# Performance work log

Measured on AMD Instinct MI355X. Metric: run time of the kernel, lower is better.

Reference implementation:

```python
import jax, jax.numpy as jnp
import numpy as np

# static problem sizes (uniform graphs -> fully vectorizable index construction)
B = 1024          # graph pairs
QS, CS, MSS = 15, 18, 20   # query size, corpus size, max_set_size
NEW = CS - QS              # nodes added to each query ('Adding' variant)
QE, CE, NE = 40, 50, QS * NEW  # edges per query / corpus / new edges per pair
D, TD = 128, 16            # node_state_dim, transform_dim
P, T = 5, 3                # n_prop_layers, n_time_updates
NPP = 2 * CS               # nodes per pair after growth (query grown to CS)
N = B * NPP                # total nodes = 36864
E = B * (QE + CE + NE)     # total edges = 138240
SINKHORN_ITERS, SINKHORN_TEMP = 10, 0.1


def setup_inputs() -> dict:
    rng = np.random.default_rng(0)
    q_off = (np.arange(B) * NPP)[:, None]
    c_off = q_off + CS
    # original query/corpus edges (already shifted to post-growth global ids)
    qf = rng.integers(0, QS, (B, QE)) + q_off
    qt = rng.integers(0, QS, (B, QE)) + q_off
    cf = rng.integers(0, CS, (B, CE)) + c_off
    ct = rng.integers(0, CS, (B, CE)) + c_off
    # new all-pairs edges existing-query-node -> new-node
    nf_ = np.tile(np.repeat(np.arange(QS), NEW), (B, 1)) + q_off
    nt_ = np.tile(np.tile(np.arange(QS, CS), QS), (B, 1)) + q_off
    from_idx = jnp.asarray(np.concatenate([qf, cf, nf_], 1).ravel(), jnp.int32)
    to_idx = jnp.asarray(np.concatenate([qt, ct, nt_], 1).ravel(), jnp.int32)
    mult_factor = jnp.asarray(
        np.concatenate([np.ones((B, QE + CE)), np.zeros((B, NE))], 1).ravel(),
        jnp.float32)
    ks = jax.random.split(jax.random.key(0), 10)
    p = lambda k, shp: jax.random.normal(k, shp, jnp.float32) * 0.05
    z = lambda n: jnp.zeros((n,), jnp.float32)
    return dict(
        node_features=jnp.ones((N, 1), jnp.float32),
        edge_features=jnp.ones((E, 1), jnp.float32),
        mult_factor=mult_factor,
        W_ne=p(ks[0], (1, D)), b_ne=z(D),
        W_ee=p(ks[1], (1, D)), b_ee=z(D),
        W_m1=p(ks[2], (3 * D, 2 * D)), b_m1=z(2 * D),
        W_m2=p(ks[3], (2 * D, D)), b_m2=z(D),
        W_u1=p(ks[4], (2 * D, 2 * D)), b_u1=z(2 * D),
        W_u2=p(ks[5], (2 * D, D)), b_u2=z(D),
        W_c1=p(ks[6], (2 * D, 2 * D)), b_c1=z(2 * D),
        W_c2=p(ks[7], (2 * D, D)), b_c2=z(D),
        W_t1=p(ks[8], (D, TD)), b_t1=z(TD),
        W_t2=p(ks[9], (TD, TD)), b_t2=z(TD),
        from_idx=from_idx, to_idx=to_idx)


def _sinkhorn(log_alpha):
    la = log_alpha / SINKHORN_TEMP
    for _ in range(SINKHORN_ITERS):
        la = la - jax.nn.logsumexp(la, axis=2, keepdims=True)
        la = la - jax.nn.logsumexp(la, axis=1, keepdims=True)
    return jnp.exp(la)


def _forward(node_features, edge_features, mult_factor,
             W_ne, b_ne, W_ee, b_ee, W_m1, b_m1, W_m2, b_m2,
             W_u1, b_u1, W_u2, b_u2, W_c1, b_c1, W_c2, b_c2,
             W_t1, b_t1, W_t2, b_t2, from_idx, to_idx):
    relu = jax.nn.relu
    nf_enc = node_features @ W_ne + b_ne          # [N, D]
    ef_enc = edge_features @ W_ee + b_ee          # [E, D]
    store = jnp.zeros((N, D * (P + 1)), nf_enc.dtype)
    qmask = (jnp.arange(MSS) < QS).astype(nf_enc.dtype)[None, :, None]
    cmask = (jnp.arange(MSS) < CS).astype(nf_enc.dtype)[None, :, None]
    for _t in range(T):
        h = nf_enc
        blocks = [jnp.zeros((N, D), nf_enc.dtype)]
        for p_ in range(1, P + 1):
            inter = store[:, D * (p_ - 1):D * p_]
            comb = relu(jnp.concatenate([h, inter], 1) @ W_c1 + b_c1) @ W_c2 + b_c2
            # GraphPropLayer: message MLP over edges, masked segment-sum aggregate
            msg_in = jnp.concatenate([comb[from_idx], comb[to_idx], ef_enc], 1)
            msg = relu(msg_in @ W_m1 + b_m1) @ W_m2 + b_m2
            msg = msg * mult_factor[:, None]      # zero out added edges
            agg = jax.ops.segment_sum(msg, to_idx, num_segments=N)
            h = relu(jnp.concatenate([comb, agg], 1) @ W_u1 + b_u1) @ W_u2 + b_u2
            blocks.append(h)
        store = jnp.concatenate(blocks, 1)        # [N, D*(P+1)]
        # pad per-graph to max_set_size and split query/corpus (interleaved)
        stacked = store.reshape(2 * B, CS, D * (P + 1))
        stacked = jnp.pad(stacked, ((0, 0), (0, MSS - CS), (0, 0)))
        q_store, c_store = stacked[0::2], stacked[1::2]   # [B, MSS, D*(P+1)]
        q_fin, c_fin = q_store[:, :, -D:], c_store[:, :, -D:]
        tq = relu(q_fin @ W_t1 + b_t1) @ W_t2 + b_t2
        tc = relu(c_fin @ W_t1 + b_t1) @ W_t2 + b_t2
        mq, mc = tq * qmask, tc * cmask
        plan = _sinkhorn(jnp.einsum('bqt,bct->bqc', mq, mc))  # [B, MSS, MSS]
        q_from_c = jnp.einsum('bqc,bcf->bqf', plan, c_store)
        c_from_q = jnp.einsum('bqc,bqf->bcf', plan, q_store)
        inter_all = jnp.stack([q_from_c, c_from_q], 1).reshape(2 * B, MSS, -1)
        store = inter_all[:, :CS, :].reshape(N, D * (P + 1))
    score = -jnp.sum(relu(mq - jnp.einsum('bqc,bct->bqt', plan, mc)), axis=(1, 2))
    return score


def reference(node_features, edge_features, mult_factor,
              W_ne, b_ne, W_ee, b_ee, W_m1, b_m1, W_m2, b_m2,
              W_u1, b_u1, W_u2, b_u2, W_c1, b_c1, W_c2, b_c2,
              W_t1, b_t1, W_t2, b_t2, from_idx, to_idx):
    return _forward(node_features, edge_features, mult_factor,
                    W_ne, b_ne, W_ee, b_ee, W_m1, b_m1, W_m2, b_m2,
                    W_u1, b_u1, W_u2, b_u2, W_c1, b_c1, W_c2, b_c2,
                    W_t1, b_t1, W_t2, b_t2, from_idx, to_idx)
```

## Files before the change

### kernel.cpp

```cpp
#include <hip/hip_runtime.h>

#define Bq   1024
#define NQS  15
#define NCS  18
#define NMSS 20
#define NPPc 36
#define NN   36864
#define DD   128
#define NTD  16
#define NP   5
#define NT   3
#define NBLK 512

typedef __attribute__((ext_vector_type(8))) short short8;
typedef __attribute__((ext_vector_type(4))) short short4v;
typedef __attribute__((ext_vector_type(4))) float float4v;

__device__ __forceinline__ short f2bf(float f) {
  unsigned u = __builtin_bit_cast(unsigned, f);
  u = u + 0x7FFFu + ((u >> 16) & 1u);
  return (short)(u >> 16);
}
__device__ __forceinline__ float bf2f(short s) {
  unsigned u = ((unsigned)(unsigned short)s) << 16;
  return __builtin_bit_cast(float, u);
}

__device__ __forceinline__ int hs_idx(int row, int col) {
  return (row << 8) + ((((col >> 3) ^ (row & 7)) << 3) | (col & 7));
}
__device__ __forceinline__ int as_idx(int row, int col) {
  return (row << 7) + ((((col >> 3) ^ (row & 7)) << 3) | (col & 7));
}
__device__ __forceinline__ int ms_idx(int f, int e) {
  return f * 104 + e;
}

#define OFF_ACT 49152
#define OFF_AGG 67584
#define OFF_UNI 86016
#define OFF_FR  122880
#define OFF_TO  123648
#define OFF_EF  124416

struct MP {
  const float* node_f; const float* edge_f;
  const int* from_idx; const int* to_idx;
  const short *WTc1, *WTm1, *WTu1, *WTc2, *WTm2, *WTu2;
  const float *b_c1, *b_c2, *b_m1, *b_m2, *b_u1, *b_u2;
  const float *c_n, *d_n, *c_e, *d_e;
  const float *W_t1, *b_t1, *W_t2, *b_t2;
  short* blkg;
  short* mixg;
  float* out;
};

template<int MT, typename F>
__device__ __forceinline__ void gemm_full(const short* __restrict__ WT, F loadB,
                                          int wm, int quad, int l16, float4v (&acc)[MT][6]) {
  short8 afr[MT][8];
#pragma unroll
  for (int ks = 0; ks < 8; ++ks)
#pragma unroll
    for (int mt = 0; mt < MT; ++mt)
      afr[mt][ks] = *(const short8*)(WT + (long)(wm * (MT * 16) + mt * 16 + l16) * 256
                                        + ks * 32 + quad * 8);
#pragma unroll
  for (int mt = 0; mt < MT; ++mt)
#pragma unroll
    for (int nt = 0; nt < 6; ++nt) acc[mt][nt] = (float4v)0.f;
#pragma unroll
  for (int ks = 0; ks < 8; ++ks) {
    const int k0q = ks * 32 + quad * 8;
    short8 bfr[6];
#pragma unroll
    for (int nt = 0; nt < 6; ++nt) bfr[nt] = loadB(nt, k0q);
#pragma unroll
    for (int mt = 0; mt < MT; ++mt)
#pragma unroll
      for (int nt = 0; nt < 6; ++nt)
        acc[mt][nt] = __builtin_amdgcn_mfma_f32_16x16x32_bf16(afr[mt][ks], bfr[nt], acc[mt][nt], 0, 0, 0);
  }
}

__global__ __launch_bounds__(512, 2) void mega(MP P) {
  __shared__ __attribute__((aligned(16))) char smem[125184];
  short* HS   = (short*)smem;
  short* actS = (short*)(smem + OFF_ACT);
  short* aggS = (short*)(smem + OFF_AGG);
  short* stgS = (short*)(smem + OFF_UNI);
  short* msgS = stgS;
  int*   frS  = (int*)(smem + OFF_FR);
  int*   toS  = (int*)(smem + OFF_TO);
  float* efS  = (float*)(smem + OFF_EF);
  float* xsS  = (float*)smem;
  float* h1S  = (float*)(smem + OFF_ACT);
  float* mqS  = (float*)(smem + OFF_AGG);
  float* mcS  = (float*)(smem + OFF_AGG + 2560);
  float* laS  = (float*)(smem + OFF_AGG + 5120);
  float* redS = (float*)(smem + OFF_AGG + 8320);
  float* wt1S = (float*)(smem + OFF_UNI);
  float* wt2S = (float*)(smem + OFF_UNI + 8192);

  const int tid = threadIdx.x, lane = tid & 63, wm = tid >> 6;
  const int quad = lane >> 4, l16 = lane & 15;
  const int b = blockIdx.x;
  const long nb = (long)b * 72;

  for (int j = tid; j < 192; j += 512) {
    int c = j / 96, jj = j - c * 96;
    if (jj < 90) {
      int e = (b * 2 + c) * 135 + jj;
      frS[j] = P.from_idx[e] - (int)nb;
      toS[j] = P.to_idx[e] - (int)nb;
      efS[j] = P.edge_f[e];
    } else { frS[j] = 0; toS[j] = -1; efS[j] = 0.f; }
  }
  __syncthreads();

  for (int t = 0; t < NT; ++t) {
    for (int p_ = (t == 0 ? 1 : 2); p_ <= NP; ++p_) {
      if (p_ == 1) {
        for (int i = tid; i < 96 * 256; i += 512) {
          int node = i >> 8, h = i & 255;
          int nc = node < 72 ? node : 71;
          float nf = P.node_f[nb + nc];
          float v = nf * P.c_n[h] + P.d_n[h] + P.b_c1[h];
          HS[hs_idx(node, h)] = f2bf(v > 0.f ? v : 0.f);
        }
        __syncthreads();
      } else {
        for (int i = tid; i < 72 * 32; i += 512) {
          int row = i >> 5, g = i & 31, col = g << 3;
          short8 v = (g < 16)
            ? *(const short8*)(P.blkg + (nb + row) * 640 + (p_ - 2) * 128 + col)
            : *(const short8*)(P.mixg + (nb + row) * 512 + (p_ - 2) * 128 + (col - 128));
          *(short8*)(&stgS[hs_idx(row, col)]) = v;
        }
        __syncthreads();
        float4v acc[2][6];
        gemm_full<2>(P.WTc1, [&](int nt, int k0q) -> short8 {
          int n = nt * 16 + l16; int nc = n < 72 ? n : 71;
          return *(const short8*)(&stgS[hs_idx(nc, k0q)]);
        }, wm, quad, l16, acc);
#pragma unroll
        for (int mt = 0; mt < 2; ++mt) {
          const int h0 = wm * 32 + mt * 16 + quad * 4;
          float4v bv = *(const float4v*)(P.b_c1 + h0);
#pragma unroll
          for (int nt = 0; nt < 6; ++nt) {
            const int col = nt * 16 + l16;
            short4v hv;
#pragma unroll
            for (int r = 0; r < 4; ++r) {
              float v = acc[mt][nt][r] + bv[r];
              hv[r] = f2bf(v > 0.f ? v : 0.f);
            }
            *(short4v*)(&HS[hs_idx(col, h0)]) = hv;
          }
        }
        __syncthreads();
      }
      {
        float4v acc2[1][6];
        gemm_full<1>(P.WTc2, [&](int nt, int k0q) -> short8 {
          return *(const short8*)(&HS[hs_idx(nt * 16 + l16, k0q)]);
        }, wm, quad, l16, acc2);
        const int f0 = wm * 16 + quad * 4;
        float4v bv = *(const float4v*)(P.b_c2 + f0);
#pragma unroll
        for (int nt = 0; nt < 6; ++nt) {
          int node = nt * 16 + l16;
          if (node < 72) {
            short4v ov;
#pragma unroll
            for (int r = 0; r < 4; ++r) ov[r] = f2bf(acc2[0][nt][r] + bv[r]);
            *(short4v*)(&actS[as_idx(node, f0)]) = ov;
          }
        }
      }
      __syncthreads();
      for (int c2 = 0; c2 < 2; ++c2) {
        int fa[6], ta[6]; float ev[6];
#pragma unroll
        for (int nt = 0; nt < 6; ++nt) {
          int j = c2 * 96 + nt * 16 + l16;
          fa[nt] = frS[j] < 0 ? 0 : frS[j];
          int tv = toS[j];
          ta[nt] = tv < 0 ? 0 : tv;
          ev[nt] = efS[j];
        }
        float4v acc[2][6];
        gemm_full<2>(P.WTm1, [&](int nt, int k0q) -> short8 {
          return (k0q < 128) ? *(const short8*)(&actS[as_idx(fa[nt], k0q)])
                             : *(const short8*)(&actS[as_idx(ta[nt], k0q - 128)]);
        }, wm, quad, l16, acc);
#pragma unroll
        for (int mt = 0; mt < 2; ++mt) {
          const int h0 = wm * 32 + mt * 16 + quad * 4;
          float4v bv = *(const float4v*)(P.b_m1 + h0);
          float4v ce = *(const float4v*)(P.c_e + h0);
          float4v de = *(const float4v*)(P.d_e + h0);
#pragma unroll
          for (int nt = 0; nt < 6; ++nt) {
            const int col = nt * 16 + l16;
            short4v hv;
#pragma unroll
            for (int r = 0; r < 4; ++r) {
              float v = acc[mt][nt][r] + bv[r] + de[r] + ev[nt] * ce[r];
              hv[r] = f2bf(v > 0.f ? v : 0.f);
            }
            *(short4v*)(&HS[hs_idx(col, h0)]) = hv;
          }
        }
        __syncthreads();
        {
          float4v acc2[1][6];
          gemm_full<1>(P.WTm2, [&](int nt, int k0q) -> short8 {
            return *(const short8*)(&HS[hs_idx(nt * 16 + l16, k0q)]);
          }, wm, quad, l16, acc2);
          const int f0 = wm * 16 + quad * 4;
          float4v bv = *(const float4v*)(P.b_m2 + f0);
#pragma unroll
          for (int nt = 0; nt < 6; ++nt) {
            int e = nt * 16 + l16;
#pragma unroll
            for (int r = 0; r < 4; ++r)
              msgS[ms_idx(f0 + r, e)] = f2bf(acc2[0][nt][r] + bv[r]);
          }
        }
        __syncthreads();
        {
          float4v ag[3];
#pragma unroll
          for (int nt = 0; nt < 3; ++nt) ag[nt] = (float4v)0.f;
          const short ONE = (short)0x3F80;
#pragma unroll
          for (int ks = 0; ks < 3; ++ks) {
            const int k0 = ks * 32 + quad * 8;
            short8 a0 = *(const short8*)(&msgS[ms_idx(wm * 16 + l16, k0)]);
            int tv[8];
#pragma unroll
            for (int j = 0; j < 8; ++j) tv[j] = toS[c2 * 96 + k0 + j];
#pragma unroll
            for (int nt = 0; nt < 3; ++nt) {
              const int node = c2 * 36 + nt * 16 + l16;
              short8 bfr;
#pragma unroll
              for (int j = 0; j < 8; ++j) bfr[j] = (tv[j] == node) ? ONE : (short)0;
              ag[nt] = __builtin_amdgcn_mfma_f32_16x16x32_bf16(a0, bfr, ag[nt], 0, 0, 0);
            }
          }
          const int f0 = wm * 16 + quad * 4;
#pragma unroll
          for (int nt = 0; nt < 3; ++nt) {
            int local = nt * 16 + l16;
            if (local < 36) {
              short4v ov;
#pragma unroll
              for (int r = 0; r < 4; ++r) ov[r] = f2bf(ag[nt][r]);
              *(short4v*)(&aggS[as_idx(c2 * 36 + local, f0)]) = ov;
            }
          }
        }
        __syncthreads();
      }
      {
        float4v acc[2][6];
        gemm_full<2>(P.WTu1, [&](int nt, int k0q) -> short8 {
          int n = nt * 16 + l16; int nc = n < 72 ? n : 71;
          return (k0q < 128) ? *(const short8*)(&actS[as_idx(nc, k0q)])
                             : *(const short8*)(&aggS[as_idx(nc, k0q - 128)]);
        }, wm, quad, l16, acc);
#pragma unroll
        for (int mt = 0; mt < 2; ++mt) {
          const int h0 = wm * 32 + mt * 16 + quad * 4;
          float4v bv = *(const float4v*)(P.b_u1 + h0);
#pragma unroll
          for (int nt = 0; nt < 6; ++nt) {
            const int col = nt * 16 + l16;
            short4v hv;
#pragma unroll
            for (int r = 0; r < 4; ++r) {
              float v = acc[mt][nt][r] + bv[r];
              hv[r] = f2bf(v > 0.f ? v : 0.f);
            }
            *(short4v*)(&HS[hs_idx(col, h0)]) = hv;
          }
        }
      }
      __syncthreads();
      {
        float4v acc2[1][6];
        gemm_full<1>(P.WTu2, [&](int nt, int k0q) -> short8 {
          return *(const short8*)(&HS[hs_idx(nt * 16 + l16, k0q)]);
        }, wm, quad, l16, acc2);
        const int f0 = wm * 16 + quad * 4;
        float4v bv = *(const float4v*)(P.b_u2 + f0);
#pragma unroll
        for (int nt = 0; nt < 6; ++nt) {
          int node = nt * 16 + l16;
          if (node < 72) {
            short4v ov;
#pragma unroll
            for (int r = 0; r < 4; ++r) ov[r] = f2bf(acc2[0][nt][r] + bv[r]);
            *(short4v*)(P.blkg + (nb + node) * 640 + (p_ - 1) * 128 + f0) = ov;
          }
        }
      }
      __syncthreads();
    }

    for (int i = tid; i < 2048; i += 512) wt1S[i] = P.W_t1[i];
    if (tid < 256) wt2S[tid] = P.W_t2[tid];
    for (int i = tid; i < 2 * NMSS * NTD; i += 512) {
      int r = (i % 320) >> 4;
      if (r >= NQS) mqS[i] = 0.f;
      if (r >= NCS) mcS[i] = 0.f;
    }
    for (int i = tid; i < 2 * 33 * 128; i += 512) {
      int r2 = i >> 7, d = i & 127;
      int bb = r2 / 33, r = r2 - bb * 33;
      long node = nb + bb * 36 + ((r < NQS) ? r : NCS + (r - NQS));
      xsS[i] = bf2f(P.blkg[node * 640 + 512 + d]);
    }
    __syncthreads();
    for (int i = tid; i < 2 * 33 * NTD; i += 512) {
      int r2 = i / NTD, c = i % NTD;
      float s = P.b_t1[c];
      for (int k = 0; k < 128; ++k) s += xsS[r2 * 128 + k] * wt1S[k * NTD + c];
      h1S[i] = s > 0.f ? s : 0.f;
    }
    __syncthreads();
    for (int i = tid; i < 2 * 33 * NTD; i += 512) {
      int r2 = i / NTD, c = i % NTD;
      int bb = r2 / 33, r = r2 - bb * 33;
      float s = P.b_t2[c];
      for (int k = 0; k < NTD; ++k) s += h1S[r2 * NTD + k] * wt2S[k * NTD + c];
      if (r < NQS) mqS[bb * 320 + r * NTD + c] = s;
      else         mcS[bb * 320 + (r - NQS) * NTD + c] = s;
    }
    __syncthreads();
    for (int i = tid; i < 800; i += 512) {
      int bb = i / 400, qc = i - bb * 400;
      int q = qc / 20, c = qc - q * 20;
      float s = 0.f;
      for (int k = 0; k < NTD; ++k) s += mqS[bb * 320 + q * NTD + k] * mcS[bb * 320 + c * NTD + k];
      laS[i] = s * 10.f;
    }
    __syncthreads();
    for (int it = 0; it < 10; ++it) {
      if (tid < 40) {
        int bb = tid / 20, q = tid - bb * 20;
        float* la = laS + bb * 400;
        float m = -1e30f;
        for (int c = 0; c < 20; ++c) m = fmaxf(m, la[q * 20 + c]);
        float s = 0.f;
        for (int c = 0; c < 20; ++c) s += expf(la[q * 20 + c] - m);
        float l = m + logf(s);
        for (int c = 0; c < 20; ++c) la[q * 20 + c] -= l;
      }
      __syncthreads();
      if (tid < 40) {
        int bb = tid / 20, c = tid - bb * 20;
        float* la = laS + bb * 400;
        float m = -1e30f;
        for (int q = 0; q < 20; ++q) m = fmaxf(m, la[q * 20 + c]);
        float s = 0.f;
        for (int q = 0; q < 20; ++q) s += expf(la[q * 20 + c] - m);
        float l = m + logf(s);
        for (int q = 0; q < 20; ++q) la[q * 20 + c] -= l;
      }
      __syncthreads();
    }
    for (int i = tid; i < 800; i += 512) laS[i] = expf(laS[i]);
    __syncthreads();
    if (t < NT - 1) {
      for (int f = tid; f < 512; f += 512) {
        for (int bb = 0; bb < 2; ++bb) {
          const float* pl = laS + bb * 400;
          long rb = nb + bb * 36;
          float oq[18], oc[18];
          for (int j = 0; j < 18; ++j) {
            oq[j] = bf2f(P.blkg[(rb + j) * 640 + f]);
            oc[j] = bf2f(P.blkg[(rb + 18 + j) * 640 + f]);
          }
          for (int j = 0; j < 18; ++j) {
            float aq = 0.f, ac = 0.f;
            for (int k = 0; k < 18; ++k) {
              aq += pl[j * 20 + k] * oc[k];
              ac += pl[k * 20 + j] * oq[k];
            }
            P.mixg[(rb + j) * 512 + f]      = f2bf(aq);
            P.mixg[(rb + 18 + j) * 512 + f] = f2bf(ac);
          }
        }
      }
      __syncthreads();
    } else {
      if (tid < 2) redS[tid] = 0.f;
      __syncthreads();
      float sl[2] = {0.f, 0.f};
      for (int i = tid; i < 640; i += 512) {
        int bb = i / 320, qt = i - bb * 320;
        int q = qt / 16, tt = qt & 15;
        float d = 0.f;
        for (int c = 0; c < 20; ++c) d += laS[bb * 400 + q * 20 + c] * mcS[bb * 320 + c * 16 + tt];
        float r = mqS[bb * 320 + qt] - d;
        if (r > 0.f) sl[bb] += r;
      }
      if (sl[0] != 0.f) atomicAdd(&redS[0], sl[0]);
      if (sl[1] != 0.f) atomicAdd(&redS[1], sl[1]);
      __syncthreads();
      if (tid < 2) P.out[b * 2 + tid] = -redS[tid];
    }
  }
}

__global__ __launch_bounds__(256) void wtrans(const float* W, short* WT, int K, int N) {
  int i = blockIdx.x * 256 + threadIdx.x;
  if (i < K * N) {
    int n = i / K, k = i - n * K;
    WT[i] = f2bf(W[(long)k * N + n]);
  }
}

__global__ __launch_bounds__(256) void consts_kernel(
    const float* W_ne, const float* b_ne, const float* W_c1,
    const float* W_ee, const float* b_ee, const float* W_m1,
    float* c_n, float* d_n, float* c_e, float* d_e) {
  int h = threadIdx.x;
  float cn = 0.f, dn = 0.f, ce = 0.f, de = 0.f;
  for (int d = 0; d < 128; ++d) {
    float wc = W_c1[d * 256 + h];
    cn += W_ne[d] * wc; dn += b_ne[d] * wc;
    float wmv = W_m1[(256 + d) * 256 + h];
    ce += W_ee[d] * wmv; de += b_ee[d] * wmv;
  }
  c_n[h] = cn; d_n[h] = dn; c_e[h] = ce; d_e[h] = de;
}

extern "C" void kernel_launch(void* const* d_in, const int* in_sizes, int n_in,
                              void* d_out, int out_size, void* d_ws, size_t ws_size,
                              hipStream_t stream) {
  (void)in_sizes; (void)n_in; (void)out_size; (void)ws_size;
  const float* node_f = (const float*)d_in[0];
  const float* edge_f = (const float*)d_in[1];
  const float* W_ne   = (const float*)d_in[3];
  const float* b_ne   = (const float*)d_in[4];
  const float* W_ee   = (const float*)d_in[5];
  const float* b_ee   = (const float*)d_in[6];
  const float* W_m1   = (const float*)d_in[7];
  const float* b_m1   = (const float*)d_in[8];
  const float* W_m2   = (const float*)d_in[9];
  const float* b_m2   = (const float*)d_in[10];
  const float* W_u1   = (const float*)d_in[11];
  const float* b_u1   = (const float*)d_in[12];
  const float* W_u2   = (const float*)d_in[13];
  const float* b_u2   = (const float*)d_in[14];
  const float* W_c1   = (const float*)d_in[15];
  const float* b_c1   = (const float*)d_in[16];
  const float* W_c2   = (const float*)d_in[17];
  const float* b_c2   = (const float*)d_in[18];
  const float* W_t1   = (const float*)d_in[19];
  const float* b_t1   = (const float*)d_in[20];
  const float* W_t2   = (const float*)d_in[21];
  const float* b_t2   = (const float*)d_in[22];
  const int* from_idx = (const int*)d_in[23];
  const int* to_idx   = (const int*)d_in[24];

  char* base = (char*)d_ws;
  size_t off = 0;
  auto alloc = [&](size_t bytes) { char* pp = base + off; off += (bytes + 255) & ~(size_t)255; return pp; };
  short* blkg = (short*)alloc((size_t)NN * 640 * 2);
  short* mixg = (short*)alloc((size_t)NN * 512 * 2);
  short* WTc1 = (short*)alloc(256 * 256 * 2);
  short* WTm1 = (short*)alloc(256 * 256 * 2);
  short* WTu1 = (short*)alloc(256 * 256 * 2);
  short* WTc2 = (short*)alloc(128 * 256 * 2);
  short* WTm2 = (short*)alloc(128 * 256 * 2);
  short* WTu2 = (short*)alloc(128 * 256 * 2);
  float* c_n  = (float*)alloc(256 * 4);
  float* d_n  = (float*)alloc(256 * 4);
  float* c_e  = (float*)alloc(256 * 4);
  float* d_e  = (float*)alloc(256 * 4);

  wtrans<<<256, 256, 0, stream>>>(W_c1, WTc1, 256, 256);
  wtrans<<<256, 256, 0, stream>>>(W_m1, WTm1, 256, 256);
  wtrans<<<256, 256, 0, stream>>>(W_u1, WTu1, 256, 256);
  wtrans<<<128, 256, 0, stream>>>(W_c2, WTc2, 256, 128);
  wtrans<<<128, 256, 0, stream>>>(W_m2, WTm2, 256, 128);
  wtrans<<<128, 256, 0, stream>>>(W_u2, WTu2, 256, 128);
  consts_kernel<<<1, 256, 0, stream>>>(W_ne, b_ne, W_c1, W_ee, b_ee, W_m1, c_n, d_n, c_e, d_e);
  hipMemsetAsync(mixg, 0, (size_t)NN * 512 * 2, stream);

  MP mp{};
  mp.node_f = node_f; mp.edge_f = edge_f;
  mp.from_idx = from_idx; mp.to_idx = to_idx;
  mp.WTc1 = WTc1; mp.WTm1 = WTm1; mp.WTu1 = WTu1;
  mp.WTc2 = WTc2; mp.WTm2 = WTm2; mp.WTu2 = WTu2;
  mp.b_c1 = b_c1; mp.b_c2 = b_c2; mp.b_m1 = b_m1; mp.b_m2 = b_m2;
  mp.b_u1 = b_u1; mp.b_u2 = b_u2;
  mp.c_n = c_n; mp.d_n = d_n; mp.c_e = c_e; mp.d_e = d_e;
  mp.W_t1 = W_t1; mp.b_t1 = b_t1; mp.W_t2 = W_t2; mp.b_t2 = b_t2;
  mp.blkg = blkg; mp.mixg = mixg; mp.out = (float*)d_out;

  mega<<<NBLK, 512, 0, stream>>>(mp);
}
```

Measured before the change: 1.644 ms.

## Keep propagation-layer staging in LDS and hoist message weight fragments to registers

Each layer's output and its cross-graph mix are now written straight into the LDS staging buffer (stgS), so the next layer no longer reloads its concatenated input from global memory. The final layer writes fp32 features for the transform MLP directly into shared memory instead of going through global bf16. The message-MLP weight fragments are loaded into registers once per kernel rather than per GEMM call, and one barrier is dropped. This cuts global traffic and barriers but raises register pressure and makes correctness depend on stgS surviving across phases that reuse the same LDS region.

```diff
diff --git a/kernel.cpp b/kernel.cpp
--- a/kernel.cpp
+++ b/kernel.cpp
@@ -42,6 +42,13 @@
 #define OFF_FR  122880
 #define OFF_TO  123648
 #define OFF_EF  124416
+#define TO_WT1  0
+#define TO_WT2  8192
+#define TO_MQ   9216
+#define TO_MC   11776
+#define TO_LA   14336
+#define TO_RED  17536
+#define TO_H1   17600
 
 struct MP {
   const float* node_f; const float* edge_f;
@@ -56,31 +63,35 @@
 };
 
 template<int MT, typename F>
-__device__ __forceinline__ void gemm_full(const short* __restrict__ WT, F loadB,
-                                          int wm, int quad, int l16, float4v (&acc)[MT][6]) {
-  short8 afr[MT][8];
+__device__ __forceinline__ void gemm_core(const short8 (&afr)[MT][8], F loadB,
+                                          int quad, float4v (&acc)[MT][6]) {
+#pragma unroll
+  for (int mt = 0; mt < MT; ++mt)
+#pragma unroll
+    for (int nt = 0; nt < 6; ++nt) acc[mt][nt] = (float4v)0.f;
+#pragma unroll
+  for (int ks = 0; ks < 8; ++ks) {
+    const int k0q = ks * 32 + quad * 8;
+    short8 bfr[6];
+#pragma unroll
+    for (int nt = 0; nt < 6; ++nt) bfr[nt] = loadB(nt, k0q);
+#pragma unroll
+    for (int mt = 0; mt < MT; ++mt)
+#pragma unroll
+      for (int nt = 0; nt < 6; ++nt)
+        acc[mt][nt] = __builtin_amdgcn_mfma_f32_16x16x32_bf16(afr[mt][ks], bfr[nt], acc[mt][nt], 0, 0, 0);
+  }
+}
+
+template<int MT>
+__device__ __forceinline__ void loadA(const short* __restrict__ WT, int wm, int quad, int l16,
+                                      short8 (&afr)[MT][8]) {
 #pragma unroll
   for (int ks = 0; ks < 8; ++ks)
 #pragma unroll
     for (int mt = 0; mt < MT; ++mt)
       afr[mt][ks] = *(const short8*)(WT + (long)(wm * (MT * 16) + mt * 16 + l16) * 256
                                         + ks * 32 + quad * 8);
-#pragma unroll
-  for (int mt = 0; mt < MT; ++mt)
-#pragma unroll
-    for (int nt = 0; nt < 6; ++nt) acc[mt][nt] = (float4v)0.f;
-#pragma unroll
-  for (int ks = 0; ks < 8; ++ks) {
-    const int k0q = ks * 32 + quad * 8;
-    short8 bfr[6];
-#pragma unroll
-    for (int nt = 0; nt < 6; ++nt) bfr[nt] = loadB(nt, k0q);
-#pragma unroll
-    for (int mt = 0; mt < MT; ++mt)
-#pragma unroll
-      for (int nt = 0; nt < 6; ++nt)
-        acc[mt][nt] = __builtin_amdgcn_mfma_f32_16x16x32_bf16(afr[mt][ks], bfr[nt], acc[mt][nt], 0, 0, 0);
-  }
 }
 
 __global__ __launch_bounds__(512, 2) void mega(MP P) {
@@ -93,19 +104,23 @@
   int*   frS  = (int*)(smem + OFF_FR);
   int*   toS  = (int*)(smem + OFF_TO);
   float* efS  = (float*)(smem + OFF_EF);
-  float* xsS  = (float*)smem;
-  float* h1S  = (float*)(smem + OFF_ACT);
-  float* mqS  = (float*)(smem + OFF_AGG);
-  float* mcS  = (float*)(smem + OFF_AGG + 2560);
-  float* laS  = (float*)(smem + OFF_AGG + 5120);
-  float* redS = (float*)(smem + OFF_AGG + 8320);
-  float* wt1S = (float*)(smem + OFF_UNI);
-  float* wt2S = (float*)(smem + OFF_UNI + 8192);
+  float* xsT  = (float*)(smem + OFF_ACT);
+  float* wt1S = (float*)(smem + TO_WT1);
+  float* wt2S = (float*)(smem + TO_WT2);
+  float* mqS  = (float*)(smem + TO_MQ);
+  float* mcS  = (float*)(smem + TO_MC);
+  float* laS  = (float*)(smem + TO_LA);
+  float* redS = (float*)(smem + TO_RED);
+  float* h1S  = (float*)(smem + TO_H1);
 
   const int tid = threadIdx.x, lane = tid & 63, wm = tid >> 6;
   const int quad = lane >> 4, l16 = lane & 15;
   const int b = blockIdx.x;
   const long nb = (long)b * 72;
+
+  short8 wm1p[2][8], wm2p[1][8];
+  loadA<2>(P.WTm1, wm, quad, l16, wm1p);
+  loadA<1>(P.WTm2, wm, quad, l16, wm2p);
 
   for (int j = tid; j < 192; j += 512) {
     int c = j / 96, jj = j - c * 96;
@@ -128,21 +143,14 @@
           float v = nf * P.c_n[h] + P.d_n[h] + P.b_c1[h];
           HS[hs_idx(node, h)] = f2bf(v > 0.f ? v : 0.f);
         }
-        __syncthreads();
       } else {
-        for (int i = tid; i < 72 * 32; i += 512) {
-          int row = i >> 5, g = i & 31, col = g << 3;
-          short8 v = (g < 16)
-            ? *(const short8*)(P.blkg + (nb + row) * 640 + (p_ - 2) * 128 + col)
-            : *(const short8*)(P.mixg + (nb + row) * 512 + (p_ - 2) * 128 + (col - 128));
-          *(short8*)(&stgS[hs_idx(row, col)]) = v;
-        }
-        __syncthreads();
+        short8 a1[2][8];
+        loadA<2>(P.WTc1, wm, quad, l16, a1);
         float4v acc[2][6];
-        gemm_full<2>(P.WTc1, [&](int nt, int k0q) -> short8 {
+        gemm_core<2>(a1, [&](int nt, int k0q) -> short8 {
           int n = nt * 16 + l16; int nc = n < 72 ? n : 71;
           return *(const short8*)(&stgS[hs_idx(nc, k0q)]);
-        }, wm, quad, l16, acc);
+        }, quad, acc);
 #pragma unroll
         for (int mt = 0; mt < 2; ++mt) {
           const int h0 = wm * 32 + mt * 16 + quad * 4;
@@ -159,13 +167,15 @@
             *(short4v*)(&HS[hs_idx(col, h0)]) = hv;
           }
         }
-        __syncthreads();
-      }
+      }
+      __syncthreads();
       {
+        short8 a2[1][8];
+        loadA<1>(P.WTc2, wm, quad, l16, a2);
         float4v acc2[1][6];
-        gemm_full<1>(P.WTc2, [&](int nt, int k0q) -> short8 {
+        gemm_core<1>(a2, [&](int nt, int k0q) -> short8 {
           return *(const short8*)(&HS[hs_idx(nt * 16 + l16, k0q)]);
-        }, wm, quad, l16, acc2);
+        }, quad, acc2);
         const int f0 = wm * 16 + quad * 4;
         float4v bv = *(const float4v*)(P.b_c2 + f0);
 #pragma unroll
@@ -180,45 +190,48 @@
         }
       }
       __syncthreads();
+#pragma unroll
       for (int c2 = 0; c2 < 2; ++c2) {
-        int fa[6], ta[6]; float ev[6];
-#pragma unroll
-        for (int nt = 0; nt < 6; ++nt) {
-          int j = c2 * 96 + nt * 16 + l16;
-          fa[nt] = frS[j] < 0 ? 0 : frS[j];
-          int tv = toS[j];
-          ta[nt] = tv < 0 ? 0 : tv;
-          ev[nt] = efS[j];
-        }
-        float4v acc[2][6];
-        gemm_full<2>(P.WTm1, [&](int nt, int k0q) -> short8 {
-          return (k0q < 128) ? *(const short8*)(&actS[as_idx(fa[nt], k0q)])
-                             : *(const short8*)(&actS[as_idx(ta[nt], k0q - 128)]);
-        }, wm, quad, l16, acc);
-#pragma unroll
-        for (int mt = 0; mt < 2; ++mt) {
-          const int h0 = wm * 32 + mt * 16 + quad * 4;
-          float4v bv = *(const float4v*)(P.b_m1 + h0);
-          float4v ce = *(const float4v*)(P.c_e + h0);
-          float4v de = *(const float4v*)(P.d_e + h0);
+        {
+          int fa[6], ta[6]; float ev[6];
 #pragma unroll
           for (int nt = 0; nt < 6; ++nt) {
-            const int col = nt * 16 + l16;
-            short4v hv;
-#pragma unroll
-            for (int r = 0; r < 4; ++r) {
-              float v = acc[mt][nt][r] + bv[r] + de[r] + ev[nt] * ce[r];
-              hv[r] = f2bf(v > 0.f ? v : 0.f);
-            }
-            *(short4v*)(&HS[hs_idx(col, h0)]) = hv;
+            int j = c2 * 96 + nt * 16 + l16;
+            fa[nt] = frS[j] < 0 ? 0 : frS[j];
+            int tv = toS[j];
+            ta[nt] = tv < 0 ? 0 : tv;
+            ev[nt] = efS[j];
+          }
+          float4v acc[2][6];
+          gemm_core<2>(wm1p, [&](int nt, int k0q) -> short8 {
+            return (k0q < 128) ? *(const short8*)(&actS[as_idx(fa[nt], k0q)])
+                               : *(const short8*)(&actS[as_idx(ta[nt], k0q - 128)]);
+          }, quad, acc);
+#pragma unroll
+          for (int mt = 0; mt < 2; ++mt) {
+            const int h0 = wm * 32 + mt * 16 + quad * 4;
+            float4v bv = *(const float4v*)(P.b_m1 + h0);
+            float4v ce = *(const float4v*)(P.c_e + h0);
+            float4v de = *(const float4v*)(P.d_e + h0);
+#pragma unroll
+            for (int nt = 0; nt < 6; ++nt) {
+              const int col = nt * 16 + l16;
+              short4v hv;
+#pragma unroll
+              for (int r = 0; r < 4; ++r) {
+                float v = acc[mt][nt][r] + bv[r] + de[r] + ev[nt] * ce[r];
+                hv[r] = f2bf(v > 0.f ? v : 0.f);
+              }
+              *(short4v*)(&HS[hs_idx(col, h0)]) = hv;
+            }
           }
         }
         __syncthreads();
         {
           float4v acc2[1][6];
-          gemm_full<1>(P.WTm2, [&](int nt, int k0q) -> short8 {
+          gemm_core<1>(wm2p, [&](int nt, int k0q) -> short8 {
             return *(const short8*)(&HS[hs_idx(nt * 16 + l16, k0q)]);
-          }, wm, quad, l16, acc2);
+          }, quad, acc2);
           const int f0 = wm * 16 + quad * 4;
           float4v bv = *(const float4v*)(P.b_m2 + f0);
 #pragma unroll
@@ -263,15 +276,25 @@
             }
           }
         }
-        __syncthreads();
+        if (c2 == 1) __syncthreads();
+        else __syncthreads();
       }
       {
+        if (p_ < 5) {
+          for (int i = tid; i < 72 * 16; i += 512) {
+            int row = i >> 4, col = (i & 15) << 3;
+            short8 v = *(const short8*)(P.mixg + (nb + row) * 512 + (p_ - 1) * 128 + col);
+            *(short8*)(&stgS[hs_idx(row, 128 + col)]) = v;
+          }
+        }
+        short8 a1[2][8];
+        loadA<2>(P.WTu1, wm, quad, l16, a1);
         float4v acc[2][6];
-        gemm_full<2>(P.WTu1, [&](int nt, int k0q) -> short8 {
+        gemm_core<2>(a1, [&](int nt, int k0q) -> short8 {
           int n = nt * 16 + l16; int nc = n < 72 ? n : 71;
           return (k0q < 128) ? *(const short8*)(&actS[as_idx(nc, k0q)])
                              : *(const short8*)(&aggS[as_idx(nc, k0q - 128)]);
-        }, wm, quad, l16, acc);
+        }, quad, acc);
 #pragma unroll
         for (int mt = 0; mt < 2; ++mt) {
           const int h0 = wm * 32 + mt * 16 + quad * 4;
@@ -291,20 +314,34 @@
       }
       __syncthreads();
       {
+        short8 a2[1][8];
+        loadA<1>(P.WTu2, wm, quad, l16, a2);
         float4v acc2[1][6];
-        gemm_full<1>(P.WTu2, [&](int nt, int k0q) -> short8 {
+        gemm_core<1>(a2, [&](int nt, int k0q) -> short8 {
           return *(const short8*)(&HS[hs_idx(nt * 16 + l16, k0q)]);
-        }, wm, quad, l16, acc2);
+        }, quad, acc2);
         const int f0 = wm * 16 + quad * 4;
         float4v bv = *(const float4v*)(P.b_u2 + f0);
 #pragma unroll
         for (int nt = 0; nt < 6; ++nt) {
           int node = nt * 16 + l16;
           if (node < 72) {
-            short4v ov;
-#pragma unroll
-            for (int r = 0; r < 4; ++r) ov[r] = f2bf(acc2[0][nt][r] + bv[r]);
-            *(short4v*)(P.blkg + (nb + node) * 640 + (p_ - 1) * 128 + f0) = ov;
+            if (p_ < 5) {
+              short4v ov;
+#pragma unroll
+              for (int r = 0; r < 4; ++r) ov[r] = f2bf(acc2[0][nt][r] + bv[r]);
+              *(short4v*)(P.blkg + (nb + node) * 640 + (p_ - 1) * 128 + f0) = ov;
+              *(short4v*)(&stgS[hs_idx(node, f0)]) = ov;
+            } else {
+              int bb = node / 36, n36 = node - bb * 36;
+              if (n36 < 15 || n36 >= 18) {
+                int row = (n36 < 15) ? n36 : n36 - 3;
+                float4v xv;
+#pragma unroll
+                for (int r = 0; r < 4; ++r) xv[r] = acc2[0][nt][r] + bv[r];
+                *(float4v*)(&xsT[(bb * 33 + row) * 128 + f0]) = xv;
+              }
+            }
           }
         }
       }
@@ -318,17 +355,11 @@
       if (r >= NQS) mqS[i] = 0.f;
       if (r >= NCS) mcS[i] = 0.f;
     }
-    for (int i = tid; i < 2 * 33 * 128; i += 512) {
-      int r2 = i >> 7, d = i & 127;
-      int bb = r2 / 33, r = r2 - bb * 33;
-      long node = nb + bb * 36 + ((r < NQS) ? r : NCS + (r - NQS));
-      xsS[i] = bf2f(P.blkg[node * 640 + 512 + d]);
-    }
     __syncthreads();
     for (int i = tid; i < 2 * 33 * NTD; i += 512) {
       int r2 = i / NTD, c = i % NTD;
       float s = P.b_t1[c];
-      for (int k = 0; k < 128; ++k) s += xsS[r2 * 128 + k] * wt1S[k * NTD + c];
+      for (int k = 0; k < 128; ++k) s += xsT[r2 * 128 + k] * wt1S[k * NTD + c];
       h1S[i] = s > 0.f ? s : 0.f;
     }
     __syncthreads();
@@ -380,10 +411,12 @@
         for (int bb = 0; bb < 2; ++bb) {
           const float* pl = laS + bb * 400;
           long rb = nb + bb * 36;
+          short rq[18], rc[18];
           float oq[18], oc[18];
           for (int j = 0; j < 18; ++j) {
-            oq[j] = bf2f(P.blkg[(rb + j) * 640 + f]);
-            oc[j] = bf2f(P.blkg[(rb + 18 + j) * 640 + f]);
+            rq[j] = P.blkg[(rb + j) * 640 + f];
+            rc[j] = P.blkg[(rb + 18 + j) * 640 + f];
+            oq[j] = bf2f(rq[j]); oc[j] = bf2f(rc[j]);
           }
           for (int j = 0; j < 18; ++j) {
             float aq = 0.f, ac = 0.f;
@@ -391,8 +424,15 @@
               aq += pl[j * 20 + k] * oc[k];
               ac += pl[k * 20 + j] * oq[k];
             }
-            P.mixg[(rb + j) * 512 + f]      = f2bf(aq);
-            P.mixg[(rb + 18 + j) * 512 + f] = f2bf(ac);
+            short hq = f2bf(aq), hc = f2bf(ac);
+            P.mixg[(rb + j) * 512 + f]      = hq;
+            P.mixg[(rb + 18 + j) * 512 + f] = hc;
+            if (f < 128) {
+              stgS[hs_idx(bb * 36 + j, f)]            = rq[j];
+              stgS[hs_idx(bb * 36 + 18 + j, f)]       = rc[j];
+              stgS[hs_idx(bb * 36 + j, 128 + f)]      = hq;
+              stgS[hs_idx(bb * 36 + 18 + j, 128 + f)] = hc;
+            }
           }
         }
       }
```

Result: slower. 2.156 ms (+31.2%).
